# Kernel tuning notes

Measured on AMD Instinct MI355X. Metric: run time of the kernel, lower is better.

## Reference

```python
import jax, jax.numpy as jnp
import numpy as np

B, D, H, E = 8192, 1024, 4096, 4
LN_EPS = 1e-5


def setup_inputs() -> dict:
    key = jax.random.key(0)
    ks = jax.random.split(key, 10)
    s_gate = 1.0 / np.sqrt(D)
    s1 = 1.0 / np.sqrt(D)
    s2 = 1.0 / np.sqrt(H)
    return {
        "x": jax.random.normal(ks[0], (B, D), dtype=jnp.float32),
        "gate_w": jax.random.uniform(ks[1], (E, D), jnp.float32, -s_gate, s_gate),
        "gate_b": jax.random.uniform(ks[2], (E,), jnp.float32, -s_gate, s_gate),
        "ln_w": jnp.ones((E, D), jnp.float32),
        "ln_b": jnp.zeros((E, D), jnp.float32),
        "w1": jax.random.uniform(ks[3], (E, D, H), jnp.float32, -s1, s1),
        "b1": jax.random.uniform(ks[4], (E, H), jnp.float32, -s1, s1),
        "w2": jax.random.uniform(ks[5], (E, H, D), jnp.float32, -s2, s2),
        "b2": jax.random.uniform(ks[6], (E, D), jnp.float32, -s2, s2),
        "top_k": 2,
    }


def reference(x, gate_w, gate_b, ln_w, ln_b, w1, b1, w2, b2, top_k):
    n_experts = gate_w.shape[0]
    # gating (eval mode: no noise)
    logits = x @ gate_w.T + gate_b            # (B, E)
    probs = jax.nn.softmax(logits, axis=-1)   # (B, E)
    top_w, top_idx = jax.lax.top_k(probs, top_k)  # (B, k)
    top_w = top_w / (jnp.sum(top_w, axis=-1, keepdims=True) + 1e-9)

    # per-expert LayerNorm: shared normalization, per-expert affine
    mu = jnp.mean(x, axis=-1, keepdims=True)
    var = jnp.var(x, axis=-1, keepdims=True)
    xn = (x - mu) * jax.lax.rsqrt(var + LN_EPS)          # (B, D)
    xe = xn[:, None, :] * ln_w[None] + ln_b[None]        # (B, E, D)

    # dense expert MLPs (GELU exact, matching torch nn.GELU default)
    h = jnp.einsum('bed,edh->beh', xe, w1) + b1[None]    # (B, E, H)
    h = jax.nn.gelu(h, approximate=False)
    stacked = jnp.einsum('beh,ehd->bed', h, w2) + b2[None]  # (B, E, D)

    # gather top-k experts and combine
    gathered = jnp.take_along_axis(stacked, top_idx[:, :, None], axis=1)  # (B, k, D)
    y = jnp.sum(gathered * top_w[:, :, None], axis=1)   # (B, D)

    # Switch load-balancing aux loss
    one_hot = jax.nn.one_hot(top_idx, n_experts, dtype=jnp.float32)  # (B, k, E)
    dispatch_frac = jnp.sum(one_hot, axis=(0, 1)) / (x.shape[0] * top_k)
    mean_prob = jnp.mean(probs, axis=0)
    aux = n_experts * jnp.sum(dispatch_frac * mean_prob)

    return y, probs, top_idx, top_w, aux
```

## Files before the change

### kernel.cpp

```cpp
#include <hip/hip_runtime.h>
#include <hip/hip_bf16.h>
#include <math.h>

#define BB 8192
#define DD 1024
#define HH 4096
#define EE 4
#define NT 132
#define CAP (NT * 128)

typedef __attribute__((ext_vector_type(8))) __bf16 bf16x8;
typedef __attribute__((ext_vector_type(4))) float f32x4;

__device__ __forceinline__ unsigned short f2bf(float f) {
    union { float f; unsigned u; } c; c.f = f;
    unsigned u = c.u;
    unsigned r = (u + 0x7FFFu + ((u >> 16) & 1u)) >> 16;
    return (unsigned short)r;
}

__device__ __forceinline__ void load_lds16(const void* g, void* l) {
    __builtin_amdgcn_global_load_lds(
        (const __attribute__((address_space(1))) void*)g,
        (__attribute__((address_space(3))) void*)l, 16, 0, 0);
}

__global__ void k_prep(const float* __restrict__ w1, const float* __restrict__ w2,
                       unsigned short* __restrict__ w1t, unsigned short* __restrict__ w2t,
                       int* __restrict__ cnt, float* __restrict__ psum,
                       int* __restrict__ done) {
    __shared__ unsigned short tileT[64 * 72];
    const int tid = threadIdx.x;
    if (blockIdx.x == 0 && blockIdx.y == 0 && blockIdx.z == 0) {
        if (tid < 4) cnt[tid] = 0;
        else if (tid < 8) psum[tid - 4] = 0.f;
        else if (tid == 8) done[0] = 0;
    }
    const int z = blockIdx.z;
    const float* s;
    unsigned short* d;
    int R, C, r0, c0;
    if (z < 4) {
        s = w1 + (size_t)z * DD * HH;  d = w1t + (size_t)z * DD * HH;
        R = DD; C = HH;
        r0 = blockIdx.y * 64; c0 = blockIdx.x * 64;
    } else {
        const int e = z - 4;
        s = w2 + (size_t)e * DD * HH;  d = w2t + (size_t)e * DD * HH;
        R = HH; C = DD;
        const int idx = blockIdx.y * 64 + blockIdx.x;
        c0 = (idx & 15) * 64; r0 = (idx >> 4) * 64;
    }
    const int cc = (tid & 15) * 4;
#pragma unroll
    for (int it = 0; it < 4; ++it) {
        int rr = (tid >> 4) + it * 16;
        float4 v = *(const float4*)(s + (size_t)(r0 + rr) * C + c0 + cc);
        tileT[(cc + 0) * 72 + rr] = f2bf(v.x);
        tileT[(cc + 1) * 72 + rr] = f2bf(v.y);
        tileT[(cc + 2) * 72 + rr] = f2bf(v.z);
        tileT[(cc + 3) * 72 + rr] = f2bf(v.w);
    }
    __syncthreads();
#pragma unroll
    for (int it = 0; it < 2; ++it) {
        int chunk = tid + it * 256;
        int cl = chunk >> 3, rl = (chunk & 7) * 8;
        uint4 vv = *(const uint4*)&tileT[cl * 72 + rl];
        *(uint4*)(d + (size_t)(c0 + cl) * R + r0 + rl) = vv;
    }
}

__global__ __launch_bounds__(256) void k_gate(
        const float* __restrict__ x, const float* __restrict__ gw,
        const float* __restrict__ gb,
        float* __restrict__ mu, float* __restrict__ rstd,
        int* __restrict__ cnt, float* __restrict__ psum, int* __restrict__ done,
        int* __restrict__ rows_tmp, float* __restrict__ wts_tmp,
        float* __restrict__ probs_out, float* __restrict__ idx_out,
        float* __restrict__ w_out,
        int* __restrict__ aoff, int* __restrict__ tile_e,
        float* __restrict__ aux_out) {
    const int tid = threadIdx.x;
    const int lane = tid & 63, wv = tid >> 6;
    __shared__ int   s_e[64];
    __shared__ float s_w[64];
    __shared__ int   s_pos[64];
    __shared__ int   s_base[4];
    __shared__ float s_ps[4][4];
    __shared__ int   s_last;

    float lp0 = 0.f, lp1 = 0.f, lp2 = 0.f, lp3 = 0.f;

    for (int i = 0; i < 8; ++i) {
        const int rloc = wv * 8 + i;
        const int r = blockIdx.x * 32 + rloc;
        float l0 = 0, l1 = 0, l2 = 0, l3 = 0, s = 0, ss = 0;
#pragma unroll
        for (int k = 0; k < 4; ++k) {
            const int off = k * 256 + lane * 4;
            float4 xv = *(const float4*)(x + (size_t)r * DD + off);
            s  += xv.x + xv.y + xv.z + xv.w;
            ss += xv.x * xv.x + xv.y * xv.y + xv.z * xv.z + xv.w * xv.w;
            float4 g0 = *(const float4*)(gw + 0 * DD + off);
            float4 g1 = *(const float4*)(gw + 1 * DD + off);
            float4 g2 = *(const float4*)(gw + 2 * DD + off);
            float4 g3 = *(const float4*)(gw + 3 * DD + off);
            l0 += xv.x * g0.x + xv.y * g0.y + xv.z * g0.z + xv.w * g0.w;
            l1 += xv.x * g1.x + xv.y * g1.y + xv.z * g1.z + xv.w * g1.w;
            l2 += xv.x * g2.x + xv.y * g2.y + xv.z * g2.z + xv.w * g2.w;
            l3 += xv.x * g3.x + xv.y * g3.y + xv.z * g3.z + xv.w * g3.w;
        }
#pragma unroll
        for (int off = 32; off > 0; off >>= 1) {
            l0 += __shfl_xor(l0, off, 64);
            l1 += __shfl_xor(l1, off, 64);
            l2 += __shfl_xor(l2, off, 64);
            l3 += __shfl_xor(l3, off, 64);
            s  += __shfl_xor(s,  off, 64);
            ss += __shfl_xor(ss, off, 64);
        }
        if (lane == 0) {
            float m = s * (1.0f / DD);
            float var = ss * (1.0f / DD) - m * m;
            mu[r] = m;
            rstd[r] = rsqrtf(var + 1e-5f);
            float lg[4] = { l0 + gb[0], l1 + gb[1], l2 + gb[2], l3 + gb[3] };
            float mx = fmaxf(fmaxf(lg[0], lg[1]), fmaxf(lg[2], lg[3]));
            float p[4], tot = 0.f;
#pragma unroll
            for (int e = 0; e < 4; ++e) { p[e] = __expf(lg[e] - mx); tot += p[e]; }
            float inv = 1.0f / tot;
#pragma unroll
            for (int e = 0; e < 4; ++e) { p[e] *= inv; probs_out[(size_t)r * 4 + e] = p[e]; }
            lp0 += p[0]; lp1 += p[1]; lp2 += p[2]; lp3 += p[3];
            int e0 = 0; float p0 = p[0];
#pragma unroll
            for (int e = 1; e < 4; ++e) if (p[e] > p0) { p0 = p[e]; e0 = e; }
            int e1 = -1; float p1 = -1.f;
#pragma unroll
            for (int e = 0; e < 4; ++e) if (e != e0 && p[e] > p1) { p1 = p[e]; e1 = e; }
            float s2 = 1.0f / (p0 + p1 + 1e-9f);
            float w0 = p0 * s2, w1v = p1 * s2;
            idx_out[r * 2 + 0] = (float)e0;
            idx_out[r * 2 + 1] = (float)e1;
            w_out[r * 2 + 0] = w0;
            w_out[r * 2 + 1] = w1v;
            s_e[rloc * 2 + 0] = e0; s_w[rloc * 2 + 0] = w0;
            s_e[rloc * 2 + 1] = e1; s_w[rloc * 2 + 1] = w1v;
        }
    }
    if (lane == 0) {
        s_ps[wv][0] = lp0; s_ps[wv][1] = lp1; s_ps[wv][2] = lp2; s_ps[wv][3] = lp3;
    }
    __syncthreads();
    if (tid < 4) {
        int c = 0;
        for (int k = 0; k < 64; ++k)
            if (s_e[k] == tid) s_pos[k] = c++;
        s_base[tid] = atomicAdd(cnt + tid, c);
        atomicAdd(psum + tid, s_ps[0][tid] + s_ps[1][tid] + s_ps[2][tid] + s_ps[3][tid]);
    }
    __syncthreads();
    if (tid < 64) {
        int e = s_e[tid];
        int p = s_base[e] + s_pos[tid];
        int r = blockIdx.x * 32 + (tid >> 1);
        rows_tmp[e * BB + p] = r;
        wts_tmp[e * BB + p] = s_w[tid];
    }
    __threadfence();
    __syncthreads();
    if (tid == 0) s_last = atomicAdd(done, 1);
    __syncthreads();
    if (s_last == (int)gridDim.x - 1 && tid == 0) {
        int c[4];
        for (int e = 0; e < 4; ++e) c[e] = atomicAdd(cnt + e, 0);
        float aux = 0.f;
        int a = 0; aoff[0] = 0;
        for (int e = 0; e < 4; ++e) {
            float mean_p = atomicAdd(psum + e, 0.f) * (1.0f / BB);
            aux += ((float)c[e] * (1.0f / (BB * 2))) * mean_p;
            a += ((c[e] + 127) >> 7) << 7; aoff[e + 1] = a;
        }
        aux_out[0] = 4.0f * aux;
        for (int t = 0; t < NT; ++t) {
            int ee = 0;
            for (int e = 0; e < 4; ++e)
                if (t * 128 >= aoff[e] && t * 128 < aoff[e + 1]) ee = e;
            tile_e[t] = ee;
        }
    }
}

__global__ __launch_bounds__(256) void k_pack(
        const float* __restrict__ x, const float* __restrict__ lnw,
        const float* __restrict__ lnb,
        const float* __restrict__ mu, const float* __restrict__ rstd,
        const int* __restrict__ cnt, const int* __restrict__ aoff,
        const int* __restrict__ tile_e,
        const int* __restrict__ rows_tmp, const float* __restrict__ wts_tmp,
        int* __restrict__ row_pk, float* __restrict__ wt_pk,
        unsigned short* __restrict__ Apk, float* __restrict__ y) {
    const int blk = blockIdx.x, tid = threadIdx.x;
    const int wv = tid >> 6, lane = tid & 63;
    if (blk < BB / 4) {
        float4 z4; z4.x = z4.y = z4.z = z4.w = 0.f;
        float* yr = y + (size_t)(blk * 4 + wv) * DD + lane * 4;
#pragma unroll
        for (int k = 0; k < 4; ++k) *(float4*)(yr + k * 256) = z4;
    }
    const int i = blk * 4 + wv;
    if (i >= aoff[4]) return;
    const int e = tile_e[i >> 7];
    const int j = i - aoff[e];
    unsigned short* dst = Apk + (size_t)i * DD;
    if (j < cnt[e]) {
        int b = rows_tmp[e * BB + j];
        if (lane == 0) { row_pk[i] = b; wt_pk[i] = wts_tmp[e * BB + j]; }
        float m = mu[b], rs = rstd[b];
#pragma unroll
        for (int k = 0; k < 4; ++k) {
            const int off = k * 256 + lane * 4;
            float4 xv = *(const float4*)(x + (size_t)b * DD + off);
            float4 wv4 = *(const float4*)(lnw + (size_t)e * DD + off);
            float4 bv4 = *(const float4*)(lnb + (size_t)e * DD + off);
            ushort4 o;
            o.x = f2bf((xv.x - m) * rs * wv4.x + bv4.x);
            o.y = f2bf((xv.y - m) * rs * wv4.y + bv4.y);
            o.z = f2bf((xv.z - m) * rs * wv4.z + bv4.z);
            o.w = f2bf((xv.w - m) * rs * wv4.w + bv4.w);
            *(ushort4*)(dst + off) = o;
        }
    } else {
        if (lane == 0) { row_pk[i] = -1; wt_pk[i] = 0.f; }
        ushort4 z; z.x = z.y = z.z = z.w = 0;
#pragma unroll
        for (int k = 0; k < 4; ++k) *(ushort4*)(dst + k * 256 + lane * 4) = z;
    }
}

template <int K, int N, int MODE>
__global__ void moe_gemm(const __bf16* __restrict__ A, const __bf16* __restrict__ W,
                         const float* __restrict__ bias,
                         const int* __restrict__ aoff, const int* __restrict__ tile_e,
                         const int* __restrict__ row_pk, const float* __restrict__ wt_pk,
                         unsigned short* __restrict__ Hout, float* __restrict__ Y) {
    __shared__ __align__(16) __bf16 As[128 * 64];
    __shared__ __align__(16) __bf16 Bs[128 * 64];

    constexpr int NBHALF = N / 128 / 2;
    constexpr int NBGRP  = (NBHALF >= 8) ? 8 : NBHALF;
    const int id = blockIdx.x;
    const int xcd = id & 7, slot = id >> 3;
    const int nbg  = slot / (33 * NBGRP);
    const int rem  = slot - nbg * (33 * NBGRP);
    const int tloc = rem / NBGRP;
    const int nbi  = rem - tloc * NBGRP;
    const int t  = (xcd >> 1) * 33 + tloc;
    const int nb = (xcd & 1) * NBHALF + nbg * NBGRP + nbi;

    if (t * 128 >= aoff[4]) return;
    const int e = tile_e[t];
    const int tid = threadIdx.x;
    const int lane = tid & 63;
    const int wave = tid >> 6;
    const int wm = wave & 1, wn = wave >> 1;
    const int lm = lane & 15, q = lane >> 4;

    const int srow = tid >> 3;
    const int schunk = ((tid & 7) ^ (srow & 7)) * 8;
    const __bf16* Ag = A + (size_t)(t * 128 + srow) * K + schunk;
    const __bf16* Bg = W + (size_t)e * N * K + (size_t)(nb * 128 + srow) * K + schunk;
    __bf16* Al = As + tid * 8;
    __bf16* Bl = Bs + tid * 8;

    f32x4 acc[4][4] = {};
    int arow[4], brow[4];
#pragma unroll
    for (int i = 0; i < 4; ++i) {
        arow[i] = wm * 64 + i * 16 + lm;
        brow[i] = wn * 64 + i * 16 + lm;
    }

    for (int kt = 0; kt < K / 64; ++kt) {
#pragma unroll
        for (int i = 0; i < 4; ++i) load_lds16(Ag + (size_t)i * 32 * K + kt * 64, Al + i * 2048);
#pragma unroll
        for (int i = 0; i < 4; ++i) load_lds16(Bg + (size_t)i * 32 * K + kt * 64, Bl + i * 2048);
        __syncthreads();
#pragma unroll
        for (int kk = 0; kk < 2; ++kk) {
            bf16x8 af[4], bfr[4];
#pragma unroll
            for (int i = 0; i < 4; ++i)
                af[i] = *(const bf16x8*)(As + arow[i] * 64 + (((kk * 4 + q) ^ (arow[i] & 7)) * 8));
#pragma unroll
            for (int j = 0; j < 4; ++j)
                bfr[j] = *(const bf16x8*)(Bs + brow[j] * 64 + (((kk * 4 + q) ^ (brow[j] & 7)) * 8));
#pragma unroll
            for (int i = 0; i < 4; ++i)
#pragma unroll
                for (int j = 0; j < 4; ++j)
                    acc[i][j] = __builtin_amdgcn_mfma_f32_16x16x32_bf16(af[i], bfr[j], acc[i][j], 0, 0, 0);
        }
        __syncthreads();
    }

    if (MODE == 1) {
#pragma unroll
        for (int j = 0; j < 4; ++j) {
            int col = nb * 128 + wn * 64 + j * 16 + lm;
            float bv = bias[e * N + col];
#pragma unroll
            for (int i = 0; i < 4; ++i) {
                int rl = wm * 64 + i * 16 + q * 4;
                size_t base = (size_t)(t * 128 + rl) * N + col;
#pragma unroll
                for (int r = 0; r < 4; ++r) {
                    float v = acc[i][j][r] + bv;
                    float u2 = 2.0f * v * (0.7978845608f + 0.0356774081f * v * v);
                    float g = v / (1.0f + __expf(-u2));
                    Hout[base + (size_t)r * N] = f2bf(g);
                }
            }
        }
    } else {
        float bv[4];
#pragma unroll
        for (int j = 0; j < 4; ++j) bv[j] = bias[e * N + nb * 128 + wn * 64 + j * 16 + lm];
#pragma unroll
        for (int i = 0; i < 4; ++i) {
#pragma unroll
            for (int r = 0; r < 4; ++r) {
                int ig = t * 128 + wm * 64 + i * 16 + q * 4 + r;
                int brw = row_pk[ig];
                if (brw >= 0) {
                    float wgt = wt_pk[ig];
#pragma unroll
                    for (int j = 0; j < 4; ++j) {
                        int col = nb * 128 + wn * 64 + j * 16 + lm;
                        atomicAdd(Y + (size_t)brw * DD + col, (acc[i][j][r] + bv[j]) * wgt);
                    }
                }
            }
        }
    }
}

extern "C" void kernel_launch(void* const* d_in, const int* in_sizes, int n_in,
                              void* d_out, int out_size, void* d_ws, size_t ws_size,
                              hipStream_t stream) {
    const float* x   = (const float*)d_in[0];
    const float* gw  = (const float*)d_in[1];
    const float* gb  = (const float*)d_in[2];
    const float* lnw = (const float*)d_in[3];
    const float* lnb = (const float*)d_in[4];
    const float* w1  = (const float*)d_in[5];
    const float* b1  = (const float*)d_in[6];
    const float* w2  = (const float*)d_in[7];
    const float* b2  = (const float*)d_in[8];
    float* out = (float*)d_out;

    char* ws = (char*)d_ws;
    size_t o = 0;
    auto alloc = [&](size_t bytes) { size_t r = o; o += (bytes + 255) & ~(size_t)255; return r; };
    float* mu       = (float*)(ws + alloc((size_t)BB * 4));
    float* rstd     = (float*)(ws + alloc((size_t)BB * 4));
    int*   cnt      = (int*)(ws + alloc(16));
    float* psum     = (float*)(ws + alloc(16));
    int*   done     = (int*)(ws + alloc(16));
    int*   aoff     = (int*)(ws + alloc(5 * 4));
    int*   te       = (int*)(ws + alloc(NT * 4));
    int*   rows_tmp = (int*)(ws + alloc((size_t)EE * BB * 4));
    float* wts_tmp  = (float*)(ws + alloc((size_t)EE * BB * 4));
    int*   row_pk   = (int*)(ws + alloc((size_t)CAP * 4));
    float* wt_pk    = (float*)(ws + alloc((size_t)CAP * 4));
    unsigned short* w1t = (unsigned short*)(ws + alloc((size_t)EE * DD * HH * 2));
    unsigned short* w2t = (unsigned short*)(ws + alloc((size_t)EE * DD * HH * 2));
    unsigned short* Apk = (unsigned short*)(ws + alloc((size_t)CAP * DD * 2));
    unsigned short* Hpk = (unsigned short*)(ws + alloc((size_t)CAP * HH * 2));
    if (o > ws_size) return;

    float* y_out     = out;
    float* probs_out = out + (size_t)BB * DD;
    float* idx_out   = probs_out + (size_t)BB * EE;
    float* w_out     = idx_out + (size_t)BB * 2;
    float* aux_out   = w_out + (size_t)BB * 2;

    k_prep<<<dim3(64, 16, 8), 256, 0, stream>>>(w1, w2, w1t, w2t, cnt, psum, done);
    k_gate<<<BB / 32, 256, 0, stream>>>(x, gw, gb, mu, rstd, cnt, psum, done,
                                        rows_tmp, wts_tmp, probs_out, idx_out, w_out,
                                        aoff, te, aux_out);
    k_pack<<<CAP / 4, 256, 0, stream>>>(x, lnw, lnb, mu, rstd, cnt, aoff, te,
                                        rows_tmp, wts_tmp, row_pk, wt_pk, Apk, y_out);
    moe_gemm<DD, HH, 1><<<8 * 33 * (HH / 256), 256, 0, stream>>>(
        (const __bf16*)Apk, (const __bf16*)w1t, b1, aoff, te, nullptr, nullptr, Hpk, nullptr);
    moe_gemm<HH, DD, 2><<<8 * 33 * (DD / 256), 256, 0, stream>>>(
        (const __bf16*)Hpk, (const __bf16*)w2t, b2, aoff, te, row_pk, wt_pk, nullptr, y_out);
}
```

Measured before the change: 650.3 us.

## Rewrite MoE GEMM with 256x256 tiles, double-buffered LDS pipeline, split-K down-projection

The expert GEMM moves from 128x128 tiles with 4 waves to 256x256 tiles with 8 waves. It double-buffers LDS and interleaves global-to-LDS loads with MFMA phases, using explicit barriers, vmcnt waits and setprio to overlap memory traffic with compute. Expert row capacity is padded to 256 and the tile count raised so tiles stay expert-aligned. The second GEMM splits K across two XCD halves and accumulates through the existing atomics, with bias added only by the first split. In exchange it uses more LDS and registers per block, pads more rows per expert, and doubles the atomic adds in the second GEMM.

```diff
diff --git a/kernel.cpp b/kernel.cpp
--- a/kernel.cpp
+++ b/kernel.cpp
@@ -6,7 +6,7 @@
 #define DD 1024
 #define HH 4096
 #define EE 4
-#define NT 132
+#define NT 136
 #define CAP (NT * 128)
 
 typedef __attribute__((ext_vector_type(8))) __bf16 bf16x8;
@@ -24,6 +24,10 @@
         (const __attribute__((address_space(1))) void*)g,
         (__attribute__((address_space(3))) void*)l, 16, 0, 0);
 }
+
+#define BARRIER() do { asm volatile("" ::: "memory"); \
+                       __builtin_amdgcn_s_barrier();  \
+                       asm volatile("" ::: "memory"); } while (0)
 
 __global__ void k_prep(const float* __restrict__ w1, const float* __restrict__ w2,
                        unsigned short* __restrict__ w1t, unsigned short* __restrict__ w2t,
@@ -181,7 +185,7 @@
         for (int e = 0; e < 4; ++e) {
             float mean_p = atomicAdd(psum + e, 0.f) * (1.0f / BB);
             aux += ((float)c[e] * (1.0f / (BB * 2))) * mean_p;
-            a += ((c[e] + 127) >> 7) << 7; aoff[e + 1] = a;
+            a += ((c[e] + 255) >> 8) << 8; aoff[e + 1] = a;
         }
         aux_out[0] = 4.0f * aux;
         for (int t = 0; t < NT; ++t) {
@@ -240,82 +244,155 @@
     }
 }
 
-template <int K, int N, int MODE>
-__global__ void moe_gemm(const __bf16* __restrict__ A, const __bf16* __restrict__ W,
-                         const float* __restrict__ bias,
-                         const int* __restrict__ aoff, const int* __restrict__ tile_e,
-                         const int* __restrict__ row_pk, const float* __restrict__ wt_pk,
-                         unsigned short* __restrict__ Hout, float* __restrict__ Y) {
-    __shared__ __align__(16) __bf16 As[128 * 64];
-    __shared__ __align__(16) __bf16 Bs[128 * 64];
-
-    constexpr int NBHALF = N / 128 / 2;
-    constexpr int NBGRP  = (NBHALF >= 8) ? 8 : NBHALF;
+template <int K, int N, int MODE, int KSPLIT>
+__global__ __launch_bounds__(512) void moe_gemm(
+        const __bf16* __restrict__ A, const __bf16* __restrict__ W,
+        const float* __restrict__ bias,
+        const int* __restrict__ aoff, const int* __restrict__ tile_e,
+        const int* __restrict__ row_pk, const float* __restrict__ wt_pk,
+        unsigned short* __restrict__ Hout, float* __restrict__ Y) {
+    __shared__ __align__(16) __bf16 As[2][256 * 64];
+    __shared__ __align__(16) __bf16 Bs[2][256 * 64];
+
+    constexpr int NBT  = N / 256;
+    constexpr int NBX  = (KSPLIT == 1) ? NBT / 2 : NBT;
+    constexpr int KSEG = K / KSPLIT;
+    constexpr int NKT  = KSEG / 64;
+
     const int id = blockIdx.x;
     const int xcd = id & 7, slot = id >> 3;
-    const int nbg  = slot / (33 * NBGRP);
-    const int rem  = slot - nbg * (33 * NBGRP);
-    const int tloc = rem / NBGRP;
-    const int nbi  = rem - tloc * NBGRP;
-    const int t  = (xcd >> 1) * 33 + tloc;
-    const int nb = (xcd & 1) * NBHALF + nbg * NBGRP + nbi;
-
-    if (t * 128 >= aoff[4]) return;
-    const int e = tile_e[t];
+    const int tloc = slot / NBX, nbi = slot % NBX;
+    const int t  = (xcd >> 1) * 17 + tloc;
+    const int nb = (KSPLIT == 1) ? (xcd & 1) * NBX + nbi : nbi;
+    const int ks = (KSPLIT == 1) ? 0 : (xcd & 1);
+
+    if (t * 256 >= aoff[4]) return;
+    const int e = tile_e[t * 2];
     const int tid = threadIdx.x;
     const int lane = tid & 63;
     const int wave = tid >> 6;
-    const int wm = wave & 1, wn = wave >> 1;
+    const int wm = wave >> 2, wn = wave & 3;
     const int lm = lane & 15, q = lane >> 4;
 
     const int srow = tid >> 3;
     const int schunk = ((tid & 7) ^ (srow & 7)) * 8;
-    const __bf16* Ag = A + (size_t)(t * 128 + srow) * K + schunk;
-    const __bf16* Bg = W + (size_t)e * N * K + (size_t)(nb * 128 + srow) * K + schunk;
-    __bf16* Al = As + tid * 8;
-    __bf16* Bl = Bs + tid * 8;
-
-    f32x4 acc[4][4] = {};
-    int arow[4], brow[4];
-#pragma unroll
-    for (int i = 0; i < 4; ++i) {
-        arow[i] = wm * 64 + i * 16 + lm;
-        brow[i] = wn * 64 + i * 16 + lm;
-    }
-
-    for (int kt = 0; kt < K / 64; ++kt) {
-#pragma unroll
-        for (int i = 0; i < 4; ++i) load_lds16(Ag + (size_t)i * 32 * K + kt * 64, Al + i * 2048);
-#pragma unroll
-        for (int i = 0; i < 4; ++i) load_lds16(Bg + (size_t)i * 32 * K + kt * 64, Bl + i * 2048);
-        __syncthreads();
-#pragma unroll
-        for (int kk = 0; kk < 2; ++kk) {
-            bf16x8 af[4], bfr[4];
+    const __bf16* Ag = A + (size_t)(t * 256 + srow) * K + ks * KSEG + schunk;
+    const __bf16* Bg = W + (size_t)e * N * K + (size_t)(nb * 256 + srow) * K + ks * KSEG + schunk;
+
+    auto stA = [&](int tile, int half) {
+        __bf16* dl = &As[tile & 1][half * 8192] + (size_t)tid * 8;
+        const __bf16* sg = Ag + (size_t)(half * 128) * K + (size_t)tile * 64;
+        load_lds16(sg, dl);
+        load_lds16(sg + (size_t)64 * K, dl + 4096);
+    };
+    auto stB = [&](int tile, int half) {
+        __bf16* dl = &Bs[tile & 1][half * 8192] + (size_t)tid * 8;
+        const __bf16* sg = Bg + (size_t)(half * 128) * K + (size_t)tile * 64;
+        load_lds16(sg, dl);
+        load_lds16(sg + (size_t)64 * K, dl + 4096);
+    };
+
+    f32x4 acc[8][4] = {};
+    bf16x8 a[8], blo[4], bhi[4];
+
+    auto rdA = [&](const __bf16* buf, int i0) {
+#pragma unroll
+        for (int i = 0; i < 4; ++i) {
+            const int r = wm * 128 + (i0 + i) * 16 + lm;
+#pragma unroll
+            for (int kk = 0; kk < 2; ++kk)
+                a[i * 2 + kk] = *(const bf16x8*)(buf + r * 64 + (((kk * 4 + q) ^ (r & 7)) * 8));
+        }
+    };
+    auto rdBlo = [&](const __bf16* buf) {
+#pragma unroll
+        for (int j = 0; j < 2; ++j) {
+            const int r = wn * 64 + j * 16 + lm;
+#pragma unroll
+            for (int kk = 0; kk < 2; ++kk)
+                blo[j * 2 + kk] = *(const bf16x8*)(buf + r * 64 + (((kk * 4 + q) ^ (r & 7)) * 8));
+        }
+    };
+    auto rdBhi = [&](const __bf16* buf) {
+#pragma unroll
+        for (int j = 0; j < 2; ++j) {
+            const int r = wn * 64 + (j + 2) * 16 + lm;
+#pragma unroll
+            for (int kk = 0; kk < 2; ++kk)
+                bhi[j * 2 + kk] = *(const bf16x8*)(buf + r * 64 + (((kk * 4 + q) ^ (r & 7)) * 8));
+        }
+    };
+    auto mma8lo = [&](int i0) {
+        __builtin_amdgcn_s_setprio(1);
+#pragma unroll
+        for (int kk = 0; kk < 2; ++kk)
 #pragma unroll
             for (int i = 0; i < 4; ++i)
-                af[i] = *(const bf16x8*)(As + arow[i] * 64 + (((kk * 4 + q) ^ (arow[i] & 7)) * 8));
-#pragma unroll
-            for (int j = 0; j < 4; ++j)
-                bfr[j] = *(const bf16x8*)(Bs + brow[j] * 64 + (((kk * 4 + q) ^ (brow[j] & 7)) * 8));
+#pragma unroll
+                for (int j = 0; j < 2; ++j)
+                    acc[i0 + i][j] = __builtin_amdgcn_mfma_f32_16x16x32_bf16(
+                        a[i * 2 + kk], blo[j * 2 + kk], acc[i0 + i][j], 0, 0, 0);
+        __builtin_amdgcn_s_setprio(0);
+    };
+    auto mma8hi = [&](int i0) {
+        __builtin_amdgcn_s_setprio(1);
+#pragma unroll
+        for (int kk = 0; kk < 2; ++kk)
 #pragma unroll
             for (int i = 0; i < 4; ++i)
 #pragma unroll
-                for (int j = 0; j < 4; ++j)
-                    acc[i][j] = __builtin_amdgcn_mfma_f32_16x16x32_bf16(af[i], bfr[j], acc[i][j], 0, 0, 0);
-        }
-        __syncthreads();
+                for (int j = 0; j < 2; ++j)
+                    acc[i0 + i][j + 2] = __builtin_amdgcn_mfma_f32_16x16x32_bf16(
+                        a[i * 2 + kk], bhi[j * 2 + kk], acc[i0 + i][j + 2], 0, 0, 0);
+        __builtin_amdgcn_s_setprio(0);
+    };
+
+    stA(0, 0); stA(0, 1); stB(0, 0); stB(0, 1);
+    if (1 < NKT) { stB(1, 0); stB(1, 1); }
+    asm volatile("s_waitcnt vmcnt(4)" ::: "memory");
+    BARRIER();
+
+#pragma unroll 1
+    for (int T = 0; T < NKT; T += 2) {
+        const __bf16* A0 = &As[0][0];
+        const __bf16* B0 = &Bs[0][0];
+        const __bf16* A1 = &As[1][0];
+        const __bf16* B1 = &Bs[1][0];
+        rdA(A0, 0); rdBlo(B0);
+        stA(T + 1, 0);
+        BARRIER(); mma8lo(0); BARRIER();
+        rdBhi(B0);
+        stA(T + 1, 1);
+        BARRIER(); mma8hi(0); BARRIER();
+        rdA(A0, 4);
+        if (T + 2 < NKT) stB(T + 2, 0);
+        BARRIER(); mma8hi(4); BARRIER();
+        if (T + 2 < NKT) { stB(T + 2, 1); asm volatile("s_waitcnt vmcnt(4)" ::: "memory"); }
+        else             { asm volatile("s_waitcnt vmcnt(0)" ::: "memory"); }
+        BARRIER(); mma8lo(4); BARRIER();
+        rdA(A1, 0); rdBlo(B1);
+        if (T + 2 < NKT) stA(T + 2, 0);
+        BARRIER(); mma8lo(0); BARRIER();
+        rdBhi(B1);
+        if (T + 2 < NKT) stA(T + 2, 1);
+        BARRIER(); mma8hi(0); BARRIER();
+        rdA(A1, 4);
+        if (T + 3 < NKT) stB(T + 3, 0);
+        BARRIER(); mma8hi(4); BARRIER();
+        if (T + 3 < NKT) { stB(T + 3, 1); asm volatile("s_waitcnt vmcnt(4)" ::: "memory"); }
+        else             { asm volatile("s_waitcnt vmcnt(0)" ::: "memory"); }
+        BARRIER(); mma8lo(4); BARRIER();
     }
 
     if (MODE == 1) {
 #pragma unroll
         for (int j = 0; j < 4; ++j) {
-            int col = nb * 128 + wn * 64 + j * 16 + lm;
-            float bv = bias[e * N + col];
-#pragma unroll
-            for (int i = 0; i < 4; ++i) {
-                int rl = wm * 64 + i * 16 + q * 4;
-                size_t base = (size_t)(t * 128 + rl) * N + col;
+            const int col = nb * 256 + wn * 64 + j * 16 + lm;
+            const float bv = bias[e * N + col];
+#pragma unroll
+            for (int i = 0; i < 8; ++i) {
+                const int rl = wm * 128 + i * 16 + q * 4;
+                const size_t base = (size_t)(t * 256 + rl) * N + col;
 #pragma unroll
                 for (int r = 0; r < 4; ++r) {
                     float v = acc[i][j][r] + bv;
@@ -328,18 +405,19 @@
     } else {
         float bv[4];
 #pragma unroll
-        for (int j = 0; j < 4; ++j) bv[j] = bias[e * N + nb * 128 + wn * 64 + j * 16 + lm];
-#pragma unroll
-        for (int i = 0; i < 4; ++i) {
+        for (int j = 0; j < 4; ++j)
+            bv[j] = (ks == 0) ? bias[e * N + nb * 256 + wn * 64 + j * 16 + lm] : 0.f;
+#pragma unroll
+        for (int i = 0; i < 8; ++i) {
 #pragma unroll
             for (int r = 0; r < 4; ++r) {
-                int ig = t * 128 + wm * 64 + i * 16 + q * 4 + r;
-                int brw = row_pk[ig];
+                const int ig = t * 256 + wm * 128 + i * 16 + q * 4 + r;
+                const int brw = row_pk[ig];
                 if (brw >= 0) {
-                    float wgt = wt_pk[ig];
+                    const float wgt = wt_pk[ig];
 #pragma unroll
                     for (int j = 0; j < 4; ++j) {
-                        int col = nb * 128 + wn * 64 + j * 16 + lm;
+                        const int col = nb * 256 + wn * 64 + j * 16 + lm;
                         atomicAdd(Y + (size_t)brw * DD + col, (acc[i][j][r] + bv[j]) * wgt);
                     }
                 }
@@ -394,8 +472,8 @@
                                         aoff, te, aux_out);
     k_pack<<<CAP / 4, 256, 0, stream>>>(x, lnw, lnb, mu, rstd, cnt, aoff, te,
                                         rows_tmp, wts_tmp, row_pk, wt_pk, Apk, y_out);
-    moe_gemm<DD, HH, 1><<<8 * 33 * (HH / 256), 256, 0, stream>>>(
+    moe_gemm<DD, HH, 1, 1><<<8 * 17 * (HH / 256 / 2), 512, 0, stream>>>(
         (const __bf16*)Apk, (const __bf16*)w1t, b1, aoff, te, nullptr, nullptr, Hpk, nullptr);
-    moe_gemm<HH, DD, 2><<<8 * 33 * (DD / 256), 256, 0, stream>>>(
+    moe_gemm<HH, DD, 2, 2><<<8 * 17 * (DD / 256), 512, 0, stream>>>(
         (const __bf16*)Hpk, (const __bf16*)w2t, b2, aoff, te, row_pk, wt_pk, nullptr, y_out);
 }
```

Result: slower. 749.4 us (+15.2%).

## Replace atomic scatter-add in second GEMM with packed bf16 output and combine kernel

Applied to the files above, without the earlier changes.

The down-projection GEMM now writes its per-slot results as bf16 into a packed buffer (reusing the A-pack buffer) instead of doing float atomicAdds into y. A new combine kernel reads each token's two expert rows through a slot-position map written during packing and forms the weighted sum directly, so y no longer needs zero-initialising. This removes heavy atomic traffic in exchange for an extra kernel launch, a round trip through a bf16 intermediate, and some loss of precision in the expert outputs.

```diff
diff --git a/kernel.cpp b/kernel.cpp
--- a/kernel.cpp
+++ b/kernel.cpp
@@ -10,6 +10,7 @@
 #define CAP (NT * 128)
 
 typedef __attribute__((ext_vector_type(8))) __bf16 bf16x8;
+typedef __attribute__((ext_vector_type(8))) unsigned short u16x8;
 typedef __attribute__((ext_vector_type(4))) float f32x4;
 
 __device__ __forceinline__ unsigned short f2bf(float f) {
@@ -17,6 +18,11 @@
     unsigned u = c.u;
     unsigned r = (u + 0x7FFFu + ((u >> 16) & 1u)) >> 16;
     return (unsigned short)r;
+}
+
+__device__ __forceinline__ float bf2f(unsigned short u) {
+    union { unsigned u; float f; } c; c.u = (unsigned)u << 16;
+    return c.f;
 }
 
 __device__ __forceinline__ void load_lds16(const void* g, void* l) {
@@ -76,7 +82,7 @@
         const float* __restrict__ gb,
         float* __restrict__ mu, float* __restrict__ rstd,
         int* __restrict__ cnt, float* __restrict__ psum, int* __restrict__ done,
-        int* __restrict__ rows_tmp, float* __restrict__ wts_tmp,
+        int* __restrict__ rows_tmp,
         float* __restrict__ probs_out, float* __restrict__ idx_out,
         float* __restrict__ w_out,
         int* __restrict__ aoff, int* __restrict__ tile_e,
@@ -84,7 +90,6 @@
     const int tid = threadIdx.x;
     const int lane = tid & 63, wv = tid >> 6;
     __shared__ int   s_e[64];
-    __shared__ float s_w[64];
     __shared__ int   s_pos[64];
     __shared__ int   s_base[4];
     __shared__ float s_ps[4][4];
@@ -146,8 +151,8 @@
             idx_out[r * 2 + 1] = (float)e1;
             w_out[r * 2 + 0] = w0;
             w_out[r * 2 + 1] = w1v;
-            s_e[rloc * 2 + 0] = e0; s_w[rloc * 2 + 0] = w0;
-            s_e[rloc * 2 + 1] = e1; s_w[rloc * 2 + 1] = w1v;
+            s_e[rloc * 2 + 0] = e0;
+            s_e[rloc * 2 + 1] = e1;
         }
     }
     if (lane == 0) {
@@ -165,9 +170,7 @@
     if (tid < 64) {
         int e = s_e[tid];
         int p = s_base[e] + s_pos[tid];
-        int r = blockIdx.x * 32 + (tid >> 1);
-        rows_tmp[e * BB + p] = r;
-        wts_tmp[e * BB + p] = s_w[tid];
+        rows_tmp[e * BB + p] = blockIdx.x * 64 + tid;
     }
     __threadfence();
     __syncthreads();
@@ -199,25 +202,19 @@
         const float* __restrict__ mu, const float* __restrict__ rstd,
         const int* __restrict__ cnt, const int* __restrict__ aoff,
         const int* __restrict__ tile_e,
-        const int* __restrict__ rows_tmp, const float* __restrict__ wts_tmp,
-        int* __restrict__ row_pk, float* __restrict__ wt_pk,
-        unsigned short* __restrict__ Apk, float* __restrict__ y) {
+        const int* __restrict__ rows_tmp,
+        int* __restrict__ pos, unsigned short* __restrict__ Apk) {
     const int blk = blockIdx.x, tid = threadIdx.x;
     const int wv = tid >> 6, lane = tid & 63;
-    if (blk < BB / 4) {
-        float4 z4; z4.x = z4.y = z4.z = z4.w = 0.f;
-        float* yr = y + (size_t)(blk * 4 + wv) * DD + lane * 4;
-#pragma unroll
-        for (int k = 0; k < 4; ++k) *(float4*)(yr + k * 256) = z4;
-    }
     const int i = blk * 4 + wv;
     if (i >= aoff[4]) return;
     const int e = tile_e[i >> 7];
     const int j = i - aoff[e];
     unsigned short* dst = Apk + (size_t)i * DD;
     if (j < cnt[e]) {
-        int b = rows_tmp[e * BB + j];
-        if (lane == 0) { row_pk[i] = b; wt_pk[i] = wts_tmp[e * BB + j]; }
+        const int v = rows_tmp[e * BB + j];
+        const int b = v >> 1;
+        if (lane == 0) pos[v] = i;
         float m = mu[b], rs = rstd[b];
 #pragma unroll
         for (int k = 0; k < 4; ++k) {
@@ -233,7 +230,6 @@
             *(ushort4*)(dst + off) = o;
         }
     } else {
-        if (lane == 0) { row_pk[i] = -1; wt_pk[i] = 0.f; }
         ushort4 z; z.x = z.y = z.z = z.w = 0;
 #pragma unroll
         for (int k = 0; k < 4; ++k) *(ushort4*)(dst + k * 256 + lane * 4) = z;
@@ -244,8 +240,7 @@
 __global__ void moe_gemm(const __bf16* __restrict__ A, const __bf16* __restrict__ W,
                          const float* __restrict__ bias,
                          const int* __restrict__ aoff, const int* __restrict__ tile_e,
-                         const int* __restrict__ row_pk, const float* __restrict__ wt_pk,
-                         unsigned short* __restrict__ Hout, float* __restrict__ Y) {
+                         unsigned short* __restrict__ Hout) {
     __shared__ __align__(16) __bf16 As[128 * 64];
     __shared__ __align__(16) __bf16 Bs[128 * 64];
 
@@ -307,44 +302,56 @@
         __syncthreads();
     }
 
-    if (MODE == 1) {
-#pragma unroll
-        for (int j = 0; j < 4; ++j) {
-            int col = nb * 128 + wn * 64 + j * 16 + lm;
-            float bv = bias[e * N + col];
-#pragma unroll
-            for (int i = 0; i < 4; ++i) {
-                int rl = wm * 64 + i * 16 + q * 4;
-                size_t base = (size_t)(t * 128 + rl) * N + col;
-#pragma unroll
-                for (int r = 0; r < 4; ++r) {
-                    float v = acc[i][j][r] + bv;
+#pragma unroll
+    for (int j = 0; j < 4; ++j) {
+        int col = nb * 128 + wn * 64 + j * 16 + lm;
+        float bv = bias[e * N + col];
+#pragma unroll
+        for (int i = 0; i < 4; ++i) {
+            int rl = wm * 64 + i * 16 + q * 4;
+            size_t base = (size_t)(t * 128 + rl) * N + col;
+#pragma unroll
+            for (int r = 0; r < 4; ++r) {
+                float v = acc[i][j][r] + bv;
+                if (MODE == 1) {
                     float u2 = 2.0f * v * (0.7978845608f + 0.0356774081f * v * v);
-                    float g = v / (1.0f + __expf(-u2));
-                    Hout[base + (size_t)r * N] = f2bf(g);
+                    v = v / (1.0f + __expf(-u2));
                 }
+                Hout[base + (size_t)r * N] = f2bf(v);
             }
         }
-    } else {
-        float bv[4];
-#pragma unroll
-        for (int j = 0; j < 4; ++j) bv[j] = bias[e * N + nb * 128 + wn * 64 + j * 16 + lm];
-#pragma unroll
-        for (int i = 0; i < 4; ++i) {
-#pragma unroll
-            for (int r = 0; r < 4; ++r) {
-                int ig = t * 128 + wm * 64 + i * 16 + q * 4 + r;
-                int brw = row_pk[ig];
-                if (brw >= 0) {
-                    float wgt = wt_pk[ig];
-#pragma unroll
-                    for (int j = 0; j < 4; ++j) {
-                        int col = nb * 128 + wn * 64 + j * 16 + lm;
-                        atomicAdd(Y + (size_t)brw * DD + col, (acc[i][j][r] + bv[j]) * wgt);
-                    }
-                }
-            }
-        }
+    }
+}
+
+__global__ __launch_bounds__(256) void k_combine(
+        const unsigned short* __restrict__ Ypk, const int* __restrict__ pos,
+        const float* __restrict__ w_out, float* __restrict__ y) {
+    const int tid = threadIdx.x;
+    const int wv = tid >> 6, lane = tid & 63;
+    const int b = blockIdx.x * 4 + wv;
+    int p0 = pos[b * 2 + 0], p1 = pos[b * 2 + 1];
+    p0 = (p0 < 0) ? 0 : (p0 >= CAP ? CAP - 1 : p0);
+    p1 = (p1 < 0) ? 0 : (p1 >= CAP ? CAP - 1 : p1);
+    const float w0 = w_out[b * 2 + 0], w1 = w_out[b * 2 + 1];
+    const unsigned short* r0 = Ypk + (size_t)p0 * DD;
+    const unsigned short* r1 = Ypk + (size_t)p1 * DD;
+    float* yr = y + (size_t)b * DD;
+#pragma unroll
+    for (int k = 0; k < 2; ++k) {
+        const int off = k * 512 + lane * 8;
+        u16x8 a = *(const u16x8*)(r0 + off);
+        u16x8 c = *(const u16x8*)(r1 + off);
+        float4 o0, o1;
+        o0.x = w0 * bf2f(a[0]) + w1 * bf2f(c[0]);
+        o0.y = w0 * bf2f(a[1]) + w1 * bf2f(c[1]);
+        o0.z = w0 * bf2f(a[2]) + w1 * bf2f(c[2]);
+        o0.w = w0 * bf2f(a[3]) + w1 * bf2f(c[3]);
+        o1.x = w0 * bf2f(a[4]) + w1 * bf2f(c[4]);
+        o1.y = w0 * bf2f(a[5]) + w1 * bf2f(c[5]);
+        o1.z = w0 * bf2f(a[6]) + w1 * bf2f(c[6]);
+        o1.w = w0 * bf2f(a[7]) + w1 * bf2f(c[7]);
+        *(float4*)(yr + off)     = o0;
+        *(float4*)(yr + off + 4) = o1;
     }
 }
 
@@ -373,13 +380,12 @@
     int*   aoff     = (int*)(ws + alloc(5 * 4));
     int*   te       = (int*)(ws + alloc(NT * 4));
     int*   rows_tmp = (int*)(ws + alloc((size_t)EE * BB * 4));
-    float* wts_tmp  = (float*)(ws + alloc((size_t)EE * BB * 4));
-    int*   row_pk   = (int*)(ws + alloc((size_t)CAP * 4));
-    float* wt_pk    = (float*)(ws + alloc((size_t)CAP * 4));
+    int*   pos      = (int*)(ws + alloc((size_t)BB * 2 * 4));
     unsigned short* w1t = (unsigned short*)(ws + alloc((size_t)EE * DD * HH * 2));
     unsigned short* w2t = (unsigned short*)(ws + alloc((size_t)EE * DD * HH * 2));
     unsigned short* Apk = (unsigned short*)(ws + alloc((size_t)CAP * DD * 2));
     unsigned short* Hpk = (unsigned short*)(ws + alloc((size_t)CAP * HH * 2));
+    unsigned short* Ypk = Apk;
     if (o > ws_size) return;
 
     float* y_out     = out;
@@ -390,12 +396,13 @@
 
     k_prep<<<dim3(64, 16, 8), 256, 0, stream>>>(w1, w2, w1t, w2t, cnt, psum, done);
     k_gate<<<BB / 32, 256, 0, stream>>>(x, gw, gb, mu, rstd, cnt, psum, done,
-                                        rows_tmp, wts_tmp, probs_out, idx_out, w_out,
+                                        rows_tmp, probs_out, idx_out, w_out,
                                         aoff, te, aux_out);
     k_pack<<<CAP / 4, 256, 0, stream>>>(x, lnw, lnb, mu, rstd, cnt, aoff, te,
-                                        rows_tmp, wts_tmp, row_pk, wt_pk, Apk, y_out);
+                                        rows_tmp, pos, Apk);
     moe_gemm<DD, HH, 1><<<8 * 33 * (HH / 256), 256, 0, stream>>>(
-        (const __bf16*)Apk, (const __bf16*)w1t, b1, aoff, te, nullptr, nullptr, Hpk, nullptr);
+        (const __bf16*)Apk, (const __bf16*)w1t, b1, aoff, te, Hpk);
     moe_gemm<HH, DD, 2><<<8 * 33 * (DD / 256), 256, 0, stream>>>(
-        (const __bf16*)Hpk, (const __bf16*)w2t, b2, aoff, te, row_pk, wt_pk, nullptr, y_out);
-}
+        (const __bf16*)Hpk, (const __bf16*)w2t, b2, aoff, te, Ypk);
+    k_combine<<<BB / 4, 256, 0, stream>>>(Ypk, pos, w_out, y_out);
+}
```

New measurement: 597.8 us. 1.09x faster.
